# Kernel tuning notes

Hardware: AMD Instinct MI355X
Metric: run time of the kernel (lower is better)

The kernel has to match this reference:

```python
import jax, jax.numpy as jnp
import numpy as np

D_MODEL = 1024
NUM_HEADS = 16
D_K = D_MODEL // NUM_HEADS
THETA = 10000.0
BATCH = 2
SEQ = 2048


def setup_inputs() -> dict:
    key = jax.random.key(0)
    ks = jax.random.split(key, 5)
    std = np.sqrt(2.0 / (D_MODEL + D_MODEL))
    return {
        "x": jax.random.normal(ks[0], (BATCH, SEQ, D_MODEL), dtype=jnp.float32),
        "Wq": jax.random.normal(ks[1], (D_MODEL, D_MODEL), dtype=jnp.float32) * std,
        "Wk": jax.random.normal(ks[2], (D_MODEL, D_MODEL), dtype=jnp.float32) * std,
        "Wv": jax.random.normal(ks[3], (D_MODEL, D_MODEL), dtype=jnp.float32) * std,
        "Wo": jax.random.normal(ks[4], (D_MODEL, D_MODEL), dtype=jnp.float32) * std,
        "token_positions": jnp.arange(SEQ, dtype=jnp.int64),
    }


def _apply_rope(t, cos, sin):
    # t: [B, H, S, D_K]; cos/sin: [S, D_K//2]
    # Block-diag 2x2 rotation on consecutive pairs (2k, 2k+1) == elementwise rotation.
    tr = t.reshape(*t.shape[:-1], D_K // 2, 2)
    t0, t1 = tr[..., 0], tr[..., 1]
    o0 = t0 * cos - t1 * sin
    o1 = t0 * sin + t1 * cos
    return jnp.stack([o0, o1], axis=-1).reshape(t.shape)


def reference(x, Wq, Wk, Wv, Wo, token_positions):
    B, S, _ = x.shape
    # projections: custom Linear does x @ W.T
    def split_heads(t):
        return t.reshape(B, S, NUM_HEADS, D_K).transpose(0, 2, 1, 3)  # [B,H,S,Dk]

    q = split_heads(x @ Wq.T)
    k = split_heads(x @ Wk.T)
    v = split_heads(x @ Wv.T)

    # RoPE angle table: theta_ik = pos / THETA**(2k/d_k)
    inv_freq = 1.0 / (THETA ** (2.0 * jnp.arange(D_K // 2, dtype=jnp.float32) / D_K))
    angles = token_positions.astype(jnp.float32)[:, None] * inv_freq[None, :]  # [S, Dk//2]
    cos, sin = jnp.cos(angles), jnp.sin(angles)

    q = _apply_rope(q, cos, sin)
    k = _apply_rope(k, cos, sin)

    scale = 1.0 / np.sqrt(D_K)
    scores = jnp.einsum("bhqd,bhkd->bhqk", q, k) * scale  # [B,H,S,S]
    causal = jnp.tril(jnp.ones((S, S), dtype=bool))
    scores = jnp.where(causal, scores, -jnp.inf)
    attn = jax.nn.softmax(scores, axis=-1)
    out = jnp.einsum("bhqk,bhkd->bhqd", attn, v)  # [B,H,S,Dk]
    out = out.transpose(0, 2, 1, 3).reshape(B, S, D_MODEL)
    return out @ Wo.T
```

## Files before the change

kernel.cpp:

```cpp
#include <hip/hip_runtime.h>
#include <hip/hip_bf16.h>
#include <cstdint>
#include <cstddef>

#define BATCH 2
#define SEQ   2048
#define DM    1024
#define NH    16
#define DK    64

typedef __attribute__((ext_vector_type(8)))  short short8;
typedef __attribute__((ext_vector_type(4)))  float f32x4;
typedef __attribute__((ext_vector_type(16))) float f32x16;
typedef __attribute__((ext_vector_type(4)))  int   i32x4;
typedef __attribute__((ext_vector_type(2)))  int   i32x2;

__device__ __forceinline__ void gload_lds16(const __hip_bfloat16* g, __hip_bfloat16* l) {
  __builtin_amdgcn_global_load_lds((const __attribute__((address_space(1))) void*)g,
                                   (__attribute__((address_space(3))) void*)l, 16, 0, 0);
}

__device__ __forceinline__ int cvtpk_bf16(float lo, float hi) {
  int r;
  asm("v_cvt_pk_bf16_f32 %0, %1, %2" : "=v"(r) : "v"(lo), "v"(hi));
  return r;
}

__device__ __forceinline__ float partner32(float x, int hi) {
  auto r = __builtin_amdgcn_permlane32_swap(__float_as_int(x), __float_as_int(x), false, false);
  return __int_as_float(hi ? r[0] : r[1]);
}

__global__ void cast_all(const float* __restrict__ x,  const float* __restrict__ Wq,
                         const float* __restrict__ Wk, const float* __restrict__ Wv,
                         const float* __restrict__ Wo, __hip_bfloat16* __restrict__ dst) {
  const int NX = BATCH * SEQ * DM;
  size_t i = ((size_t)blockIdx.x * 256 + threadIdx.x) * 4;
  const float* s;
  if (i < (size_t)NX) {
    s = x + i;
  } else {
    size_t j = i - NX;
    int wsel = (int)(j >> 20);
    size_t o = j & ((1u << 20) - 1);
    s = (wsel == 0 ? Wq : wsel == 1 ? Wk : wsel == 2 ? Wv : Wo) + o;
  }
  float4 v = *(const float4*)s;
  i32x2 pk;
  pk[0] = cvtpk_bf16(v.x, v.y);
  pk[1] = cvtpk_bf16(v.z, v.w);
  *(i32x2*)(dst + i) = pk;
}

template<bool F32OUT, bool VSPLIT>
__global__ __launch_bounds__(256)
void gemm_bt(const __hip_bfloat16* __restrict__ A,
             const __hip_bfloat16* __restrict__ Bw,
             void* __restrict__ Cv, __hip_bfloat16* __restrict__ vt,
             int M, int N, int K, int ldc) {
  __shared__ __hip_bfloat16 As[128 * 32];
  __shared__ __hip_bfloat16 Bs[128 * 32];
  const int tid  = threadIdx.x;
  const int lane = tid & 63;
  const int w    = tid >> 6;
  const int wr   = w >> 1, wc = w & 1;
  const int g    = lane >> 4;
  const int lr   = lane & 15;
  const int bm0  = blockIdx.y * 128;
  const int bn0  = blockIdx.x * 128;

  f32x4 acc[4][4] = {};

  const int strow = lane >> 2;
  const int stcol = (lane & 3) * 8;

  for (int kt = 0; kt < K; kt += 32) {
    #pragma unroll
    for (int it = 0; it < 2; ++it) {
      int c   = w * 2 + it;
      int row = c * 16 + strow;
      gload_lds16(A  + (size_t)(bm0 + row) * K + kt + stcol, As + row * 32 + stcol);
      gload_lds16(Bw + (size_t)(bn0 + row) * K + kt + stcol, Bs + row * 32 + stcol);
    }
    __syncthreads();
    short8 a[4], b[4];
    #pragma unroll
    for (int m = 0; m < 4; ++m)
      a[m] = *(const short8*)(As + (wr * 64 + m * 16 + lr) * 32 + g * 8);
    #pragma unroll
    for (int n = 0; n < 4; ++n)
      b[n] = *(const short8*)(Bs + (wc * 64 + n * 16 + lr) * 32 + g * 8);
    #pragma unroll
    for (int m = 0; m < 4; ++m)
      #pragma unroll
      for (int n = 0; n < 4; ++n)
        acc[m][n] = __builtin_amdgcn_mfma_f32_16x16x32_bf16(a[m], b[n], acc[m][n], 0, 0, 0);
    __syncthreads();
  }

  if (VSPLIT && bn0 >= 2048) {
    #pragma unroll
    for (int m = 0; m < 4; ++m)
      #pragma unroll
      for (int n = 0; n < 4; ++n) {
        int nn = bn0 + wc * 64 + n * 16 + lr - 2048;
        int hd = nn >> 6, d = nn & 63;
        int m0 = bm0 + wr * 64 + m * 16 + g * 4;
        int bb = m0 >> 11, ss = m0 & 2047;
        i32x2 pk;
        pk[0] = cvtpk_bf16(acc[m][n][0], acc[m][n][1]);
        pk[1] = cvtpk_bf16(acc[m][n][2], acc[m][n][3]);
        *(i32x2*)(vt + ((size_t)(bb * NH + hd) * DK + d) * SEQ + ss) = pk;
      }
  } else {
    #pragma unroll
    for (int m = 0; m < 4; ++m)
      #pragma unroll
      for (int n = 0; n < 4; ++n) {
        int col = bn0 + wc * 64 + n * 16 + lr;
        #pragma unroll
        for (int r = 0; r < 4; ++r) {
          int row = bm0 + wr * 64 + m * 16 + g * 4 + r;
          float v = acc[m][n][r];
          if (F32OUT) ((float*)Cv)[(size_t)row * ldc + col] = v;
          else        ((__hip_bfloat16*)Cv)[(size_t)row * ldc + col] = __float2bfloat16(v);
        }
      }
  }
}

__global__ void rope_kernel(__hip_bfloat16* __restrict__ qk, const int* __restrict__ pos) {
  int idx = blockIdx.x * 256 + threadIdx.x;
  if (idx >= BATCH * SEQ * NH * (DK / 2)) return;
  int m  = idx >> 9;
  int hp = idx & 511;
  int h  = hp >> 5;
  int pk = hp & 31;
  int s  = m & (SEQ - 1);
  float p   = (float)pos[s];
  float ang = p * exp2f(-(float)pk * 0.415241011860920f);
  float cv, sv;
  __sincosf(ang, &sv, &cv);
  const float QS = 0.125f * 1.4426950408889634f;
  size_t base = (size_t)m * 2048 + h * DK + 2 * pk;
  float q0 = __bfloat162float(qk[base]),          q1 = __bfloat162float(qk[base + 1]);
  qk[base]     = __float2bfloat16((q0 * cv - q1 * sv) * QS);
  qk[base + 1] = __float2bfloat16((q0 * sv + q1 * cv) * QS);
  float k0 = __bfloat162float(qk[base + 1024]),   k1 = __bfloat162float(qk[base + 1025]);
  qk[base + 1024] = __float2bfloat16(k0 * cv - k1 * sv);
  qk[base + 1025] = __float2bfloat16(k0 * sv + k1 * cv);
}

__global__ __launch_bounds__(512)
void flash_attn(const __hip_bfloat16* __restrict__ qk,
                const __hip_bfloat16* __restrict__ vt,
                __hip_bfloat16* __restrict__ outb) {
  __shared__ __hip_bfloat16 Kls[2][64 * 64];
  __shared__ __hip_bfloat16 Vls[2][64 * 64];
  const int pi = blockIdx.x;
  const int NQB = SEQ / 128;
  const int qbh = NQB - 1 - pi, qbl = pi;
  const int hd = blockIdx.y, b = blockIdx.z;
  const int tid = threadIdx.x, lane = tid & 63, w = tid >> 6;
  const int wh = w & 3;
  const int qb_eff = (w < 4) ? qbh : qbl;
  const int hi = lane >> 5, ql = lane & 31;
  const int q0w = qb_eff * 128 + wh * 32;
  const int nt  = 2 * qbh + 2;
  const int tmaxw = 2 * qb_eff + (wh >> 1);

  const __hip_bfloat16* Qb = qk + (size_t)(b * SEQ) * 2048 + hd * DK;
  const __hip_bfloat16* Kg = qk + (size_t)(b * SEQ) * 2048 + 1024 + hd * DK;
  const __hip_bfloat16* Vg = vt + (size_t)(b * NH + hd) * DK * SEQ;

  short8 qf[4];
  #pragma unroll
  for (int c = 0; c < 4; ++c)
    qf[c] = *(const short8*)(Qb + (size_t)(q0w + ql) * 2048 + c * 16 + hi * 8);

  f32x16 o0 = {}, o1 = {};
  float m_run = -1e30f, l_run = 0.f;

  const int srow = tid >> 3;
  const int sc0  = (tid & 7) * 8;
  const int swz  = (srow & 7) << 3;

  short8 kr, vr;
  kr = *(const short8*)(Kg + (size_t)srow * 2048 + sc0);
  vr = *(const short8*)(Vg + (size_t)srow * SEQ + sc0);
  *(short8*)(&Kls[0][srow * 64 + (sc0 ^ swz)]) = kr;
  *(short8*)(&Vls[0][srow * 64 + (sc0 ^ swz)]) = vr;

  for (int t = 0; t < nt; ++t) {
    const int cur = t & 1;
    if (t + 1 < nt) {
      int r0 = (t + 1) * 64;
      kr = *(const short8*)(Kg + (size_t)(r0 + srow) * 2048 + sc0);
      vr = *(const short8*)(Vg + (size_t)srow * SEQ + r0 + sc0);
    }
    __syncthreads();

    if (t <= tmaxw) {
      f32x16 s0 = {}, s1 = {};
      __builtin_amdgcn_s_setprio(1);
      #pragma unroll
      for (int c = 0; c < 4; ++c) {
        int col = (c * 16 + hi * 8) ^ ((ql & 7) << 3);
        short8 ka = *(const short8*)(&Kls[cur][ql * 64 + col]);
        short8 kb = *(const short8*)(&Kls[cur][(32 + ql) * 64 + col]);
        s0 = __builtin_amdgcn_mfma_f32_32x32x16_bf16(ka, qf[c], s0, 0, 0, 0);
        s1 = __builtin_amdgcn_mfma_f32_32x32x16_bf16(kb, qf[c], s1, 0, 0, 0);
      }
      __builtin_amdgcn_s_setprio(0);

      if (t * 64 + 63 > q0w) {
        int qg = q0w + ql;
        #pragma unroll
        for (int r = 0; r < 16; ++r) {
          int krow = (r & 3) + 8 * (r >> 2) + 4 * hi;
          if (t * 64 + krow > qg)      s0[r] = -1e30f;
          if (t * 64 + 32 + krow > qg) s1[r] = -1e30f;
        }
      }

      float mx = s0[0];
      #pragma unroll
      for (int r = 1; r < 16; ++r) mx = fmaxf(mx, s0[r]);
      #pragma unroll
      for (int r = 0; r < 16; ++r) mx = fmaxf(mx, s1[r]);
      mx = fmaxf(mx, partner32(mx, hi));

      if (!__all(mx <= m_run + 8.f)) {
        float mn  = fmaxf(m_run, mx);
        float fac = __builtin_amdgcn_exp2f(m_run - mn);
        m_run = mn;
        l_run *= fac;
        #pragma unroll
        for (int r = 0; r < 16; ++r) { o0[r] *= fac; o1[r] *= fac; }
      }
      float sum = 0.f;
      #pragma unroll
      for (int r = 0; r < 16; ++r) { s0[r] = __builtin_amdgcn_exp2f(s0[r] - m_run); sum += s0[r]; }
      #pragma unroll
      for (int r = 0; r < 16; ++r) { s1[r] = __builtin_amdgcn_exp2f(s1[r] - m_run); sum += s1[r]; }
      sum += partner32(sum, hi);
      l_run += sum;

      short8 pf[4];
      #pragma unroll
      for (int kt = 0; kt < 2; ++kt) {
        const f32x16& sv = kt ? s1 : s0;
        #pragma unroll
        for (int u = 0; u < 2; ++u) {
          int wa0 = cvtpk_bf16(sv[8 * u + 0], sv[8 * u + 1]);
          int wa1 = cvtpk_bf16(sv[8 * u + 2], sv[8 * u + 3]);
          int wb0 = cvtpk_bf16(sv[8 * u + 4], sv[8 * u + 5]);
          int wb1 = cvtpk_bf16(sv[8 * u + 6], sv[8 * u + 7]);
          auto r0 = __builtin_amdgcn_permlane32_swap(wa0, wb0, false, false);
          auto r1 = __builtin_amdgcn_permlane32_swap(wa1, wb1, false, false);
          i32x4 fr; fr[0] = r0[0]; fr[1] = r1[0]; fr[2] = r0[1]; fr[3] = r1[1];
          pf[kt * 2 + u] = *(short8*)&fr;
        }
      }

      __builtin_amdgcn_s_setprio(1);
      #pragma unroll
      for (int cc = 0; cc < 4; ++cc) {
        int col = (cc * 16 + hi * 8) ^ ((ql & 7) << 3);
        short8 va = *(const short8*)(&Vls[cur][ql * 64 + col]);
        short8 vb = *(const short8*)(&Vls[cur][(32 + ql) * 64 + col]);
        o0 = __builtin_amdgcn_mfma_f32_32x32x16_bf16(va, pf[cc], o0, 0, 0, 0);
        o1 = __builtin_amdgcn_mfma_f32_32x32x16_bf16(vb, pf[cc], o1, 0, 0, 0);
      }
      __builtin_amdgcn_s_setprio(0);
    }

    if (t + 1 < nt) {
      const int nxt = cur ^ 1;
      *(short8*)(&Kls[nxt][srow * 64 + (sc0 ^ swz)]) = kr;
      *(short8*)(&Vls[nxt][srow * 64 + (sc0 ^ swz)]) = vr;
    }
  }

  float inv = 1.f / l_run;
  __hip_bfloat16* orow = outb + (size_t)(b * SEQ + q0w + ql) * DM + hd * DK;
  #pragma unroll
  for (int dt = 0; dt < 2; ++dt) {
    const f32x16& oa = dt ? o1 : o0;
    #pragma unroll
    for (int a = 0; a < 4; ++a) {
      int d0 = dt * 32 + a * 8 + hi * 4;
      i32x2 pk;
      pk[0] = cvtpk_bf16(oa[4 * a + 0] * inv, oa[4 * a + 1] * inv);
      pk[1] = cvtpk_bf16(oa[4 * a + 2] * inv, oa[4 * a + 3] * inv);
      *(i32x2*)(orow + d0) = pk;
    }
  }
}

extern "C" void kernel_launch(void* const* d_in, const int* in_sizes, int n_in,
                              void* d_out, int out_size, void* d_ws, size_t ws_size,
                              hipStream_t stream) {
  const float* x  = (const float*)d_in[0];
  const float* Wq = (const float*)d_in[1];
  const float* Wk = (const float*)d_in[2];
  const float* Wv = (const float*)d_in[3];
  const float* Wo = (const float*)d_in[4];
  const int*   tp = (const int*)d_in[5];
  float* out = (float*)d_out;

  char* ws = (char*)d_ws;
  __hip_bfloat16* xb    = (__hip_bfloat16*)(ws);
  __hip_bfloat16* wqkv  = (__hip_bfloat16*)(ws + (8u  << 20));
  __hip_bfloat16* wob   = (__hip_bfloat16*)(ws + (14u << 20));
  __hip_bfloat16* qkbuf = (__hip_bfloat16*)(ws + (16u << 20));
  __hip_bfloat16* vtbuf = (__hip_bfloat16*)(ws + (32u << 20));
  __hip_bfloat16* attnb = (__hip_bfloat16*)(ws + (40u << 20));

  cast_all<<<8192, 256, 0, stream>>>(x, Wq, Wk, Wv, Wo, xb);

  gemm_bt<false, true><<<dim3(3 * DM / 128, BATCH * SEQ / 128), 256, 0, stream>>>(
      xb, wqkv, (void*)qkbuf, vtbuf, BATCH * SEQ, 3 * DM, DM, 2048);

  rope_kernel<<<(BATCH * SEQ * NH * (DK / 2)) / 256, 256, 0, stream>>>(qkbuf, tp);

  flash_attn<<<dim3(SEQ / 256, NH, BATCH), 512, 0, stream>>>(qkbuf, vtbuf, attnb);

  gemm_bt<true, false><<<dim3(DM / 128, BATCH * SEQ / 128), 256, 0, stream>>>(
      attnb, wob, (void*)out, nullptr, BATCH * SEQ, DM, DM, DM);
}
```

Measured before the change: 125.4 us.

## Fuse RoPE into QKV GEMM epilogue and switch to 32x32x16 MFMA tiles

Removes the separate RoPE kernel by applying the rotation and Q scaling in the QKV GEMM epilogue, using a lane shuffle to fetch each element's pair partner. This saves a full read-modify-write pass over the Q/K buffer and one kernel launch. It also changes the GEMM inner loop from 16x16x32 to 32x32x16 MFMA, with a k-group-major LDS layout, which cuts LDS fragment loads per MFMA. In exchange, the epilogue now computes sincos per element, which is redundant across heads and output tiles, and it also writes Q/K with scalar bf16 stores.

```diff
diff --git a/kernel.cpp b/kernel.cpp
--- a/kernel.cpp
+++ b/kernel.cpp
@@ -57,98 +57,108 @@
 void gemm_bt(const __hip_bfloat16* __restrict__ A,
              const __hip_bfloat16* __restrict__ Bw,
              void* __restrict__ Cv, __hip_bfloat16* __restrict__ vt,
+             const int* __restrict__ pos,
              int M, int N, int K, int ldc) {
-  __shared__ __hip_bfloat16 As[128 * 32];
-  __shared__ __hip_bfloat16 Bs[128 * 32];
+  __shared__ __hip_bfloat16 As[4 * 128 * 8];
+  __shared__ __hip_bfloat16 Bs[4 * 128 * 8];
   const int tid  = threadIdx.x;
   const int lane = tid & 63;
   const int w    = tid >> 6;
   const int wr   = w >> 1, wc = w & 1;
-  const int g    = lane >> 4;
-  const int lr   = lane & 15;
+  const int hi   = lane >> 5;
+  const int ql   = lane & 31;
   const int bm0  = blockIdx.y * 128;
   const int bn0  = blockIdx.x * 128;
 
-  f32x4 acc[4][4] = {};
-
-  const int strow = lane >> 2;
-  const int stcol = (lane & 3) * 8;
+  f32x16 acc[2][2] = {};
 
   for (int kt = 0; kt < K; kt += 32) {
     #pragma unroll
-    for (int it = 0; it < 2; ++it) {
-      int c   = w * 2 + it;
-      int row = c * 16 + strow;
-      gload_lds16(A  + (size_t)(bm0 + row) * K + kt + stcol, As + row * 32 + stcol);
-      gload_lds16(Bw + (size_t)(bn0 + row) * K + kt + stcol, Bs + row * 32 + stcol);
+    for (int c = 0; c < 2; ++c) {
+      int s  = c * 256 + w * 64 + lane;
+      int gA = s >> 7, mA = s & 127;
+      gload_lds16(A  + (size_t)(bm0 + mA) * K + kt + gA * 8, As + (size_t)(gA * 128 + mA) * 8);
+      gload_lds16(Bw + (size_t)(bn0 + mA) * K + kt + gA * 8, Bs + (size_t)(gA * 128 + mA) * 8);
     }
     __syncthreads();
-    short8 a[4], b[4];
-    #pragma unroll
-    for (int m = 0; m < 4; ++m)
-      a[m] = *(const short8*)(As + (wr * 64 + m * 16 + lr) * 32 + g * 8);
-    #pragma unroll
-    for (int n = 0; n < 4; ++n)
-      b[n] = *(const short8*)(Bs + (wc * 64 + n * 16 + lr) * 32 + g * 8);
-    #pragma unroll
-    for (int m = 0; m < 4; ++m)
-      #pragma unroll
-      for (int n = 0; n < 4; ++n)
-        acc[m][n] = __builtin_amdgcn_mfma_f32_16x16x32_bf16(a[m], b[n], acc[m][n], 0, 0, 0);
+
+    short8 a[2][2], b[2][2];
+    #pragma unroll
+    for (int ks = 0; ks < 2; ++ks) {
+      int g = ks * 2 + hi;
+      #pragma unroll
+      for (int mq = 0; mq < 2; ++mq)
+        a[mq][ks] = *(const short8*)(As + (size_t)(g * 128 + wr * 64 + mq * 32 + ql) * 8);
+      #pragma unroll
+      for (int nq = 0; nq < 2; ++nq)
+        b[nq][ks] = *(const short8*)(Bs + (size_t)(g * 128 + wc * 64 + nq * 32 + ql) * 8);
+    }
+    #pragma unroll
+    for (int ks = 0; ks < 2; ++ks)
+      #pragma unroll
+      for (int mq = 0; mq < 2; ++mq)
+        #pragma unroll
+        for (int nq = 0; nq < 2; ++nq)
+          acc[mq][nq] = __builtin_amdgcn_mfma_f32_32x32x16_bf16(a[mq][ks], b[nq][ks], acc[mq][nq], 0, 0, 0);
     __syncthreads();
   }
 
   if (VSPLIT && bn0 >= 2048) {
     #pragma unroll
-    for (int m = 0; m < 4; ++m)
-      #pragma unroll
-      for (int n = 0; n < 4; ++n) {
-        int nn = bn0 + wc * 64 + n * 16 + lr - 2048;
+    for (int mq = 0; mq < 2; ++mq)
+      #pragma unroll
+      for (int nq = 0; nq < 2; ++nq) {
+        int nn = bn0 + wc * 64 + nq * 32 + ql - 2048;
         int hd = nn >> 6, d = nn & 63;
-        int m0 = bm0 + wr * 64 + m * 16 + g * 4;
-        int bb = m0 >> 11, ss = m0 & 2047;
-        i32x2 pk;
-        pk[0] = cvtpk_bf16(acc[m][n][0], acc[m][n][1]);
-        pk[1] = cvtpk_bf16(acc[m][n][2], acc[m][n][3]);
-        *(i32x2*)(vt + ((size_t)(bb * NH + hd) * DK + d) * SEQ + ss) = pk;
+        #pragma unroll
+        for (int rg = 0; rg < 4; ++rg) {
+          int s0 = bm0 + wr * 64 + mq * 32 + rg * 8 + hi * 4;
+          int bb = s0 >> 11, ss = s0 & 2047;
+          i32x2 pk;
+          pk[0] = cvtpk_bf16(acc[mq][nq][rg * 4 + 0], acc[mq][nq][rg * 4 + 1]);
+          pk[1] = cvtpk_bf16(acc[mq][nq][rg * 4 + 2], acc[mq][nq][rg * 4 + 3]);
+          *(i32x2*)(vt + ((size_t)(bb * NH + hd) * DK + d) * SEQ + ss) = pk;
+        }
+      }
+  } else if (VSPLIT) {
+    const bool isQ = (bn0 < 1024);
+    const float qsc = isQ ? 0.125f * 1.4426950408889634f : 1.0f;
+    #pragma unroll
+    for (int mq = 0; mq < 2; ++mq)
+      #pragma unroll
+      for (int nq = 0; nq < 2; ++nq) {
+        int col = bn0 + wc * 64 + nq * 32 + ql;
+        int d   = col & 63;
+        int odd = d & 1;
+        float invf = exp2f(-(float)(d >> 1) * 0.415241011860920f);
+        #pragma unroll
+        for (int r = 0; r < 16; ++r) {
+          int row = bm0 + wr * 64 + mq * 32 + (r & 3) + 8 * (r >> 2) + 4 * hi;
+          float own  = acc[mq][nq][r];
+          float part = __shfl_xor(own, 1, 64);
+          float p    = (float)pos[row & (SEQ - 1)];
+          float ang  = p * invf;
+          float sv, cv;
+          __sincosf(ang, &sv, &cv);
+          float val = odd ? (part * sv + own * cv) : (own * cv - part * sv);
+          ((__hip_bfloat16*)Cv)[(size_t)row * ldc + col] = __float2bfloat16(val * qsc);
+        }
       }
   } else {
     #pragma unroll
-    for (int m = 0; m < 4; ++m)
-      #pragma unroll
-      for (int n = 0; n < 4; ++n) {
-        int col = bn0 + wc * 64 + n * 16 + lr;
-        #pragma unroll
-        for (int r = 0; r < 4; ++r) {
-          int row = bm0 + wr * 64 + m * 16 + g * 4 + r;
-          float v = acc[m][n][r];
+    for (int mq = 0; mq < 2; ++mq)
+      #pragma unroll
+      for (int nq = 0; nq < 2; ++nq) {
+        int col = bn0 + wc * 64 + nq * 32 + ql;
+        #pragma unroll
+        for (int r = 0; r < 16; ++r) {
+          int row = bm0 + wr * 64 + mq * 32 + (r & 3) + 8 * (r >> 2) + 4 * hi;
+          float v = acc[mq][nq][r];
           if (F32OUT) ((float*)Cv)[(size_t)row * ldc + col] = v;
           else        ((__hip_bfloat16*)Cv)[(size_t)row * ldc + col] = __float2bfloat16(v);
         }
       }
   }
-}
-
-__global__ void rope_kernel(__hip_bfloat16* __restrict__ qk, const int* __restrict__ pos) {
-  int idx = blockIdx.x * 256 + threadIdx.x;
-  if (idx >= BATCH * SEQ * NH * (DK / 2)) return;
-  int m  = idx >> 9;
-  int hp = idx & 511;
-  int h  = hp >> 5;
-  int pk = hp & 31;
-  int s  = m & (SEQ - 1);
-  float p   = (float)pos[s];
-  float ang = p * exp2f(-(float)pk * 0.415241011860920f);
-  float cv, sv;
-  __sincosf(ang, &sv, &cv);
-  const float QS = 0.125f * 1.4426950408889634f;
-  size_t base = (size_t)m * 2048 + h * DK + 2 * pk;
-  float q0 = __bfloat162float(qk[base]),          q1 = __bfloat162float(qk[base + 1]);
-  qk[base]     = __float2bfloat16((q0 * cv - q1 * sv) * QS);
-  qk[base + 1] = __float2bfloat16((q0 * sv + q1 * cv) * QS);
-  float k0 = __bfloat162float(qk[base + 1024]),   k1 = __bfloat162float(qk[base + 1025]);
-  qk[base + 1024] = __float2bfloat16(k0 * cv - k1 * sv);
-  qk[base + 1025] = __float2bfloat16(k0 * sv + k1 * cv);
 }
 
 __global__ __launch_bounds__(512)
@@ -320,12 +330,10 @@
   cast_all<<<8192, 256, 0, stream>>>(x, Wq, Wk, Wv, Wo, xb);
 
   gemm_bt<false, true><<<dim3(3 * DM / 128, BATCH * SEQ / 128), 256, 0, stream>>>(
-      xb, wqkv, (void*)qkbuf, vtbuf, BATCH * SEQ, 3 * DM, DM, 2048);
-
-  rope_kernel<<<(BATCH * SEQ * NH * (DK / 2)) / 256, 256, 0, stream>>>(qkbuf, tp);
+      xb, wqkv, (void*)qkbuf, vtbuf, tp, BATCH * SEQ, 3 * DM, DM, 2048);
 
   flash_attn<<<dim3(SEQ / 256, NH, BATCH), 512, 0, stream>>>(qkbuf, vtbuf, attnb);
 
   gemm_bt<true, false><<<dim3(DM / 128, BATCH * SEQ / 128), 256, 0, stream>>>(
-      attnb, wob, (void*)out, nullptr, BATCH * SEQ, DM, DM, DM);
-}
+      attnb, wob, (void*)out, nullptr, nullptr, BATCH * SEQ, DM, DM, DM);
+}
```

Result: slower. 154.5 us (+23.1%).

## Fuse RoPE into QKV GEMM epilogue and swizzle GEMM LDS tiles

Applied to the files above, without the earlier changes.

Removes the standalone RoPE kernel. The cos/sin table is now computed inside the cast kernel, and the rotation plus Q scaling are applied in the QKV GEMM epilogue, using a lane shuffle to fetch the partner element. This drops one full read-modify-write pass over the Q/K buffer and one kernel launch. It also adds an XOR swizzle to the GEMM shared-memory tiles to reduce LDS bank conflicts on the fragment loads. The table reuses the attention output buffer region, which is only safe because attention writes that region after the GEMM has consumed the table.

```diff
diff --git a/kernel.cpp b/kernel.cpp
--- a/kernel.cpp
+++ b/kernel.cpp
@@ -8,6 +8,7 @@
 #define DM    1024
 #define NH    16
 #define DK    64
+#define LOG2E 1.4426950408889634f
 
 typedef __attribute__((ext_vector_type(8)))  short short8;
 typedef __attribute__((ext_vector_type(4)))  float f32x4;
@@ -33,9 +34,18 @@
 
 __global__ void cast_all(const float* __restrict__ x,  const float* __restrict__ Wq,
                          const float* __restrict__ Wk, const float* __restrict__ Wv,
-                         const float* __restrict__ Wo, __hip_bfloat16* __restrict__ dst) {
+                         const float* __restrict__ Wo, __hip_bfloat16* __restrict__ dst,
+                         const int* __restrict__ pos,  float2* __restrict__ tbl) {
   const int NX = BATCH * SEQ * DM;
-  size_t i = ((size_t)blockIdx.x * 256 + threadIdx.x) * 4;
+  int t = blockIdx.x * 256 + threadIdx.x;
+  if (t < SEQ * 32) {
+    int s = t >> 5, d2 = t & 31;
+    float ang = (float)pos[s] * exp2f(-(float)d2 * 0.415241011860920f);
+    float cv, sv;
+    __sincosf(ang, &sv, &cv);
+    tbl[t] = make_float2(cv, sv);
+  }
+  size_t i = (size_t)t * 4;
   const float* s;
   if (i < (size_t)NX) {
     s = x + i;
@@ -57,6 +67,7 @@
 void gemm_bt(const __hip_bfloat16* __restrict__ A,
              const __hip_bfloat16* __restrict__ Bw,
              void* __restrict__ Cv, __hip_bfloat16* __restrict__ vt,
+             const float2* __restrict__ tbl,
              int M, int N, int K, int ldc) {
   __shared__ __hip_bfloat16 As[128 * 32];
   __shared__ __hip_bfloat16 Bs[128 * 32];
@@ -72,24 +83,28 @@
   f32x4 acc[4][4] = {};
 
   const int strow = lane >> 2;
-  const int stcol = (lane & 3) * 8;
-
+  const int stc   = lane & 3;
   for (int kt = 0; kt < K; kt += 32) {
     #pragma unroll
     for (int it = 0; it < 2; ++it) {
       int c   = w * 2 + it;
       int row = c * 16 + strow;
-      gload_lds16(A  + (size_t)(bm0 + row) * K + kt + stcol, As + row * 32 + stcol);
-      gload_lds16(Bw + (size_t)(bn0 + row) * K + kt + stcol, Bs + row * 32 + stcol);
+      int csrc = stc ^ (row & 3);
+      gload_lds16(A  + (size_t)(bm0 + row) * K + kt + csrc * 8, As + row * 32 + stc * 8);
+      gload_lds16(Bw + (size_t)(bn0 + row) * K + kt + csrc * 8, Bs + row * 32 + stc * 8);
     }
     __syncthreads();
     short8 a[4], b[4];
     #pragma unroll
-    for (int m = 0; m < 4; ++m)
-      a[m] = *(const short8*)(As + (wr * 64 + m * 16 + lr) * 32 + g * 8);
-    #pragma unroll
-    for (int n = 0; n < 4; ++n)
-      b[n] = *(const short8*)(Bs + (wc * 64 + n * 16 + lr) * 32 + g * 8);
+    for (int m = 0; m < 4; ++m) {
+      int row = wr * 64 + m * 16 + lr;
+      a[m] = *(const short8*)(As + row * 32 + ((g ^ (row & 3)) << 3));
+    }
+    #pragma unroll
+    for (int n = 0; n < 4; ++n) {
+      int row = wc * 64 + n * 16 + lr;
+      b[n] = *(const short8*)(Bs + row * 32 + ((g ^ (row & 3)) << 3));
+    }
     #pragma unroll
     for (int m = 0; m < 4; ++m)
       #pragma unroll
@@ -112,6 +127,26 @@
         pk[1] = cvtpk_bf16(acc[m][n][2], acc[m][n][3]);
         *(i32x2*)(vt + ((size_t)(bb * NH + hd) * DK + d) * SEQ + ss) = pk;
       }
+  } else if (VSPLIT) {
+    const bool isQ = (bn0 < 1024);
+    const float qsc = isQ ? 0.125f * LOG2E : 1.0f;
+    #pragma unroll
+    for (int m = 0; m < 4; ++m)
+      #pragma unroll
+      for (int n = 0; n < 4; ++n) {
+        int col = bn0 + wc * 64 + n * 16 + lr;
+        int d   = col & 63;
+        int odd = d & 1, d2 = d >> 1;
+        #pragma unroll
+        for (int r = 0; r < 4; ++r) {
+          int row = bm0 + wr * 64 + m * 16 + g * 4 + r;
+          float own  = acc[m][n][r];
+          float part = __shfl_xor(own, 1, 64);
+          float2 cs  = tbl[(row & (SEQ - 1)) * 32 + d2];
+          float val  = odd ? (part * cs.y + own * cs.x) : (own * cs.x - part * cs.y);
+          ((__hip_bfloat16*)Cv)[(size_t)row * ldc + col] = __float2bfloat16(val * qsc);
+        }
+      }
   } else {
     #pragma unroll
     for (int m = 0; m < 4; ++m)
@@ -127,28 +162,6 @@
         }
       }
   }
-}
-
-__global__ void rope_kernel(__hip_bfloat16* __restrict__ qk, const int* __restrict__ pos) {
-  int idx = blockIdx.x * 256 + threadIdx.x;
-  if (idx >= BATCH * SEQ * NH * (DK / 2)) return;
-  int m  = idx >> 9;
-  int hp = idx & 511;
-  int h  = hp >> 5;
-  int pk = hp & 31;
-  int s  = m & (SEQ - 1);
-  float p   = (float)pos[s];
-  float ang = p * exp2f(-(float)pk * 0.415241011860920f);
-  float cv, sv;
-  __sincosf(ang, &sv, &cv);
-  const float QS = 0.125f * 1.4426950408889634f;
-  size_t base = (size_t)m * 2048 + h * DK + 2 * pk;
-  float q0 = __bfloat162float(qk[base]),          q1 = __bfloat162float(qk[base + 1]);
-  qk[base]     = __float2bfloat16((q0 * cv - q1 * sv) * QS);
-  qk[base + 1] = __float2bfloat16((q0 * sv + q1 * cv) * QS);
-  float k0 = __bfloat162float(qk[base + 1024]),   k1 = __bfloat162float(qk[base + 1025]);
-  qk[base + 1024] = __float2bfloat16(k0 * cv - k1 * sv);
-  qk[base + 1025] = __float2bfloat16(k0 * sv + k1 * cv);
 }
 
 __global__ __launch_bounds__(512)
@@ -316,16 +329,15 @@
   __hip_bfloat16* qkbuf = (__hip_bfloat16*)(ws + (16u << 20));
   __hip_bfloat16* vtbuf = (__hip_bfloat16*)(ws + (32u << 20));
   __hip_bfloat16* attnb = (__hip_bfloat16*)(ws + (40u << 20));
-
-  cast_all<<<8192, 256, 0, stream>>>(x, Wq, Wk, Wv, Wo, xb);
+  float2*         tbl   = (float2*)(ws + (40u << 20));
+
+  cast_all<<<8192, 256, 0, stream>>>(x, Wq, Wk, Wv, Wo, xb, tp, tbl);
 
   gemm_bt<false, true><<<dim3(3 * DM / 128, BATCH * SEQ / 128), 256, 0, stream>>>(
-      xb, wqkv, (void*)qkbuf, vtbuf, BATCH * SEQ, 3 * DM, DM, 2048);
-
-  rope_kernel<<<(BATCH * SEQ * NH * (DK / 2)) / 256, 256, 0, stream>>>(qkbuf, tp);
+      xb, wqkv, (void*)qkbuf, vtbuf, tbl, BATCH * SEQ, 3 * DM, DM, 2048);
 
   flash_attn<<<dim3(SEQ / 256, NH, BATCH), 512, 0, stream>>>(qkbuf, vtbuf, attnb);
 
   gemm_bt<true, false><<<dim3(DM / 128, BATCH * SEQ / 128), 256, 0, stream>>>(
-      attnb, wob, (void*)out, nullptr, BATCH * SEQ, DM, DM, DM);
-}
+      attnb, wob, (void*)out, nullptr, nullptr, BATCH * SEQ, DM, DM, DM);
+}
```

Result: slower. 128.5 us (+2.5%).
